# Optimization experiments

Measured on AMD Instinct MI355X. Metric: run time of the kernel, lower is better.

## Reference

```python
import jax, jax.numpy as jnp
import numpy as np


def silu(v):
    return v * jax.nn.sigmoid(v)


def setup_inputs() -> dict:
    key = jax.random.key(0)
    ks = jax.random.split(key, 9)
    B, L, d_model = 2, 2048, 1024
    expand, d_state, d_conv = 2, 16, 4
    d_inner = expand * d_model          # 2048
    dt_rank = (d_model + 15) // 16      # 64 (ceil(d_model/16))
    sc = 0.02
    s = lambda k, shape: (jax.random.normal(k, shape, jnp.float32) * sc)
    A_init = jnp.tile(jnp.arange(1, d_state + 1, dtype=jnp.float32), (d_inner, 1))
    return {
        "x": jax.random.normal(ks[0], (B, L, d_model), jnp.float32),
        "in_proj_w": s(ks[1], (2 * d_inner, d_model)),
        "conv_w": s(ks[2], (d_inner, 1, d_conv)),
        "conv_b": s(ks[3], (d_inner,)),
        "x_proj_w": s(ks[4], (dt_rank + 2 * d_state, d_inner)),
        "dt_proj_w": s(ks[5], (d_inner, dt_rank)),
        "dt_proj_b": s(ks[6], (d_inner,)),
        "A_log": jnp.log(A_init),
        "D": jnp.ones((d_inner,), jnp.float32),
        "out_proj_w": s(ks[7], (d_model, d_inner)),
    }


def _mamba(x, in_proj_w, conv_w, conv_b, x_proj_w, dt_proj_w, dt_proj_b, A_log, D, out_proj_w):
    Bsz, L, d_model = x.shape
    d_inner, _, d_conv = conv_w.shape
    d_state = A_log.shape[1]
    dt_rank = dt_proj_w.shape[1]

    # input projection -> [B, L, 2*d_inner], split into conv branch and gate
    xz = jnp.einsum('bld,ed->ble', x, in_proj_w)
    x_in, z = jnp.split(xz, 2, axis=-1)

    # causal depthwise conv1d over sequence
    xt = jnp.transpose(x_in, (0, 2, 1))                      # [B, d_inner, L]
    xt = jnp.pad(xt, ((0, 0), (0, 0), (d_conv - 1, 0)))
    xc = jax.lax.conv_general_dilated(
        xt, conv_w, window_strides=(1,), padding='VALID',
        dimension_numbers=('NCH', 'OIH', 'NCH'),
        feature_group_count=d_inner)
    xc = xc + conv_b[None, :, None]
    u = silu(jnp.transpose(xc, (0, 2, 1)))                   # [B, L, d_inner]

    # ssm parameter projections
    x_dbl = jnp.einsum('ble,fe->blf', u, x_proj_w)           # [B, L, dt_rank + 2*d_state]
    dt, B_ssm, C_ssm = jnp.split(x_dbl, [dt_rank, dt_rank + d_state], axis=-1)
    delta = jax.nn.softplus(jnp.einsum('blr,er->ble', dt, dt_proj_w) + dt_proj_b)  # [B,L,d_inner]
    A = -jnp.exp(A_log)                                       # [d_inner, d_state]

    # selective scan: h_t = exp(delta_t * A) * h_{t-1} + delta_t * u_t * B_t
    def step(h, inp):
        d_t, B_t, C_t, u_t = inp                              # [B,e],[B,n],[B,n],[B,e]
        dA = jnp.exp(d_t[..., None] * A)                      # [B, d_inner, d_state]
        h = dA * h + (d_t * u_t)[..., None] * B_t[:, None, :]
        y = jnp.einsum('ben,bn->be', h, C_t)
        return h, y

    h0 = jnp.zeros((Bsz, d_inner, d_state), x.dtype)
    scan_in = (jnp.swapaxes(delta, 0, 1), jnp.swapaxes(B_ssm, 0, 1),
               jnp.swapaxes(C_ssm, 0, 1), jnp.swapaxes(u, 0, 1))
    _, ys = jax.lax.scan(step, h0, scan_in)                   # ys: [L, B, d_inner]
    y = jnp.swapaxes(ys, 0, 1) + u * D                        # skip term D*u

    y = y * silu(z)                                           # gate
    return jnp.einsum('ble,de->bld', y, out_proj_w)


def reference(x, in_proj_w, conv_w, conv_b, x_proj_w, dt_proj_w, dt_proj_b, A_log, D, out_proj_w):
    # ResidualMamba: x + Mamba(x)
    return x + _mamba(x, in_proj_w, conv_w, conv_b, x_proj_w,
                      dt_proj_w, dt_proj_b, A_log, D, out_proj_w)
```

## Files before the change

kernel.cpp:

```cpp
#include <hip/hip_runtime.h>
#include <hip/hip_bf16.h>
#include <math.h>

typedef __bf16 bf16;
typedef __attribute__((ext_vector_type(8))) __bf16 bf16x8;
typedef __attribute__((ext_vector_type(4))) __bf16 bf16x4;
typedef __attribute__((ext_vector_type(4))) float  f32x4;

static constexpr int Bsz = 2, L = 2048, DM = 1024, DI = 2048, DS = 16, DTR = 64;
static constexpr int M   = Bsz * L;
static constexpr int NXZ = 2 * DI;
static constexpr int NXD = DTR + 2 * DS;
static constexpr int NC  = 32;
static constexpr int CL  = L / NC;
static constexpr int KS  = 8;
static constexpr float LOG2E = 1.4426950408889634f;

__device__ inline float ex2(float x) { return __builtin_amdgcn_exp2f(x); }

__device__ inline void gload_lds16(const void* g, void* l)
{
    __builtin_amdgcn_global_load_lds(
        (const __attribute__((address_space(1))) void*)g,
        (__attribute__((address_space(3))) void*)l, 16, 0, 0);
}

#define SBAR() { asm volatile("" ::: "memory"); __builtin_amdgcn_s_barrier(); asm volatile("" ::: "memory"); }
#define VMCNT4() asm volatile("s_waitcnt vmcnt(4)" ::: "memory")
#define VMCNT0() asm volatile("s_waitcnt vmcnt(0)" ::: "memory")

static constexpr int C0 = M * DM / 4;
static constexpr int C1 = C0 + NXZ * DM / 4;
static constexpr int C2 = C1 + DM * DI / 4;
static constexpr int C3 = C2 + NXD * DI / 4;
static constexpr int C4 = C3 + DI * DTR / 4;

__global__ __launch_bounds__(256)
void cast_all(const float* __restrict__ s0, const float* __restrict__ s1,
              const float* __restrict__ s2, const float* __restrict__ s3,
              const float* __restrict__ s4,
              bf16* __restrict__ d0, bf16* __restrict__ d1,
              bf16* __restrict__ d2, bf16* __restrict__ d3,
              bf16* __restrict__ d4)
{
    const int i = blockIdx.x * 256 + threadIdx.x;
    const float* s; bf16* d; int off;
    if      (i < C0) { s = s0; d = d0; off = 0;  }
    else if (i < C1) { s = s1; d = d1; off = C0; }
    else if (i < C2) { s = s2; d = d2; off = C1; }
    else if (i < C3) { s = s3; d = d3; off = C2; }
    else             { s = s4; d = d4; off = C3; }
    const int j = i - off;
    float4 v = ((const float4*)s)[j];
    bf16x4 o = {(bf16)v.x, (bf16)v.y, (bf16)v.z, (bf16)v.w};
    ((bf16x4*)d)[j] = o;
}

static constexpr int GK  = DM;
static constexpr int GNT = GK / 64;

__device__ __forceinline__ void stage_half(const bf16* __restrict__ Gbase, int ld,
                                           int kbase, bf16* lds_slot, int tid, int wid)
{
    const int rl = tid >> 2;
    const int ks = ((tid & 3) ^ (rl & 3)) << 3;
#pragma unroll
    for (int i = 0; i < 2; ++i)
        gload_lds16(Gbase + (size_t)(i * 128 + rl) * ld + kbase + ks,
                    lds_slot + i * 4096 + wid * 512);
}

template<int MH>
__device__ __forceinline__ void ldA4(const bf16* As, int abase, bf16x8 af[4])
{
#pragma unroll
    for (int mm = 0; mm < 4; ++mm)
        af[mm] = *(const bf16x8*)(As + abase + (MH * 4 + mm) * 512);
}

__device__ __forceinline__ void ldB4(const bf16* Bs, int bbase, bf16x8 bfr[4])
{
#pragma unroll
    for (int nn = 0; nn < 4; ++nn)
        bfr[nn] = *(const bf16x8*)(Bs + bbase + nn * 512);
}

template<int MH>
__device__ __forceinline__ void mfma16(f32x4 acc[8][4], const bf16x8 af[4],
                                       const bf16x8 bfr[4])
{
#pragma unroll
    for (int mm = 0; mm < 4; ++mm)
#pragma unroll
        for (int nn = 0; nn < 4; ++nn)
            acc[MH * 4 + mm][nn] = __builtin_amdgcn_mfma_f32_16x16x32_bf16(
                af[mm], bfr[nn], acc[MH * 4 + mm][nn], 0, 0, 0);
}

__global__ __launch_bounds__(512, 1)
void gemm256_inproj(const bf16* __restrict__ A, const bf16* __restrict__ Bw,
                    bf16* __restrict__ C)
{
    __shared__ __align__(16) bf16 Asl[4 * 8192];
    __shared__ __align__(16) bf16 Bsl[4 * 8192];

    const int tid  = threadIdx.x;
    const int wid  = tid >> 6;
    const int lane = tid & 63;
    const int wr   = wid >> 2;
    const int wc   = wid & 3;
    const int fr   = lane & 15;
    const int ko16 = lane >> 4;
    const int kx   = ((ko16 ^ (fr & 3)) << 3);

    const int bid = blockIdx.x;
    const int wg  = (bid & 7) * 32 + (bid >> 3);
    const int by  = wg >> 4, bx = wg & 15;
    const int row0 = by * 256, col0 = bx * 256;

    const bf16* Ablk = A  + (size_t)row0 * GK;
    const bf16* Bblk = Bw + (size_t)col0 * GK;

    const int abase = (wr * 128 + fr) * 32 + kx;
    const int bbase = (wc * 64 + fr) * 32 + kx;

    f32x4 acc[8][4] = {};
    bf16x8 af[4], bfr[4];

    stage_half(Ablk, GK, 0,       Asl + 0 * 8192, tid, wid);
    stage_half(Bblk, GK, 0,       Bsl + 0 * 8192, tid, wid);
    stage_half(Ablk, GK, 32,      Asl + 1 * 8192, tid, wid);
    stage_half(Bblk, GK, 32,      Bsl + 1 * 8192, tid, wid);
    stage_half(Ablk, GK, 64,      Asl + 2 * 8192, tid, wid);
    stage_half(Bblk, GK, 64,      Bsl + 2 * 8192, tid, wid);
    VMCNT4();
    SBAR();

    for (int t = 0; t < GNT; ++t) {
        const int sk0 = (2 * t) & 3, sk1 = (2 * t + 1) & 3;
        const bf16* As0 = Asl + sk0 * 8192;
        const bf16* As1 = Asl + sk1 * 8192;
        const bf16* Bs0 = Bsl + sk0 * 8192;
        const bf16* Bs1 = Bsl + sk1 * 8192;

        ldA4<0>(As0, abase, af);
        ldB4(Bs0, bbase, bfr);
        if (t + 1 < GNT)
            stage_half(Ablk, GK, (t + 1) * 64 + 32, Asl + ((2 * t + 3) & 3) * 8192, tid, wid);
        SBAR();
        __builtin_amdgcn_s_setprio(1);
        mfma16<0>(acc, af, bfr);
        __builtin_amdgcn_s_setprio(0);
        SBAR();

        ldA4<1>(As0, abase, af);
        if (t + 1 < GNT)
            stage_half(Bblk, GK, (t + 1) * 64 + 32, Bsl + ((2 * t + 3) & 3) * 8192, tid, wid);
        SBAR();
        __builtin_amdgcn_s_setprio(1);
        mfma16<1>(acc, af, bfr);
        __builtin_amdgcn_s_setprio(0);
        SBAR();

        ldA4<0>(As1, abase, af);
        ldB4(Bs1, bbase, bfr);
        if (t + 2 < GNT)
            stage_half(Ablk, GK, (t + 2) * 64, Asl + sk0 * 8192, tid, wid);
        SBAR();
        __builtin_amdgcn_s_setprio(1);
        mfma16<0>(acc, af, bfr);
        __builtin_amdgcn_s_setprio(0);
        SBAR();

        ldA4<1>(As1, abase, af);
        if (t + 2 < GNT)
            stage_half(Bblk, GK, (t + 2) * 64, Bsl + sk0 * 8192, tid, wid);
        SBAR();
        __builtin_amdgcn_s_setprio(1);
        mfma16<1>(acc, af, bfr);
        __builtin_amdgcn_s_setprio(0);
        if (t < GNT - 3) { VMCNT4(); } else { VMCNT0(); }
        SBAR();
    }

    const int r0 = row0 + wr * 128 + (ko16 << 2);
    const int c0 = col0 + wc * 64 + fr;
#pragma unroll
    for (int m = 0; m < 8; ++m)
#pragma unroll
        for (int n = 0; n < 4; ++n)
#pragma unroll
            for (int r = 0; r < 4; ++r)
                C[(size_t)(r0 + m * 16 + r) * NXZ + c0 + n * 16] = (bf16)acc[m][n][r];
}

__global__ __launch_bounds__(256)
void gemm_out(const bf16* __restrict__ A, const bf16* __restrict__ Bw,
              const float* __restrict__ res, float* __restrict__ Cout)
{
    __shared__ __align__(16) bf16 Asl[128 * 32];
    __shared__ __align__(16) bf16 Bsl[64 * 32];

    const int tid  = threadIdx.x;
    const int bid  = blockIdx.x;
    const int orig = (bid & 7) * 64 + (bid >> 3);
    const int bx   = orig & 15;
    const int by   = orig >> 4;
    const int row0 = by * 128, col0 = bx * 64;

    const int w    = tid >> 6;
    const int lane = tid & 63;
    const int wr   = w >> 1, wc = w & 1;
    const int fr   = lane & 15;
    const int ko   = (lane >> 4) << 3;

    f32x4 acc[4][2] = {};

    const int sr = tid >> 2;
    const int sk = (tid & 3) << 3;
    const bf16* gA0 = A  + (size_t)(row0 + sr) * NXZ + sk;
    const bf16* gA1 = A  + (size_t)(row0 + 64 + sr) * NXZ + sk;
    const bf16* gB0 = Bw + (size_t)(col0 + sr) * DI + sk;
    char* lA = (char*)Asl + w * 1024;
    char* lB = (char*)Bsl + w * 1024;

    for (int k0 = 0; k0 < DI; k0 += 32) {
        gload_lds16(gA0 + k0, lA);
        gload_lds16(gA1 + k0, lA + 4096);
        gload_lds16(gB0 + k0, lB);
        __syncthreads();

        bf16x8 af[4], bfr[2];
#pragma unroll
        for (int m = 0; m < 4; ++m)
            af[m] = *(const bf16x8*)&Asl[((wr << 6) + m * 16 + fr) * 32 + ko];
#pragma unroll
        for (int n = 0; n < 2; ++n)
            bfr[n] = *(const bf16x8*)&Bsl[((wc << 5) + n * 16 + fr) * 32 + ko];
#pragma unroll
        for (int m = 0; m < 4; ++m)
#pragma unroll
            for (int n = 0; n < 2; ++n)
                acc[m][n] = __builtin_amdgcn_mfma_f32_16x16x32_bf16(
                    af[m], bfr[n], acc[m][n], 0, 0, 0);
        __syncthreads();
    }

    const int r0 = row0 + (wr << 6) + ((lane >> 4) << 2);
    const int c0 = col0 + (wc << 5) + fr;
#pragma unroll
    for (int m = 0; m < 4; ++m)
#pragma unroll
        for (int n = 0; n < 2; ++n)
#pragma unroll
            for (int r = 0; r < 4; ++r) {
                const int row = r0 + m * 16 + r;
                const int col = c0 + n * 16;
                Cout[(size_t)row * DM + col] =
                    acc[m][n][r] + res[(size_t)row * DM + col];
            }
}

template<int EPI>
__global__ __launch_bounds__(256)
void gemm_bf16(const bf16* __restrict__ A, const bf16* __restrict__ Bw,
               const float* __restrict__ bias, const float* __restrict__ res,
               void* __restrict__ Cout, int N, int K, int lda, int ldc)
{
    __shared__ __align__(16) bf16 Asl[128 * 32];
    __shared__ __align__(16) bf16 Bsl[128 * 32];

    const int tid  = threadIdx.x;
    const int row0 = blockIdx.y * 128;
    const int col0 = blockIdx.x * 128;
    const int w    = tid >> 6;
    const int lane = tid & 63;
    const int wr   = w >> 1, wc = w & 1;
    const int fr   = lane & 15;
    const int ko   = (lane >> 4) << 3;

    f32x4 acc[4][4] = {};

    const int sr = tid >> 2;
    const int sk = (tid & 3) << 3;
    int brow0 = col0 + sr;       if (brow0 > N - 1) brow0 = N - 1;
    int brow1 = col0 + 64 + sr;  if (brow1 > N - 1) brow1 = N - 1;
    const bf16* gA0 = A  + (size_t)(row0 + sr) * lda + sk;
    const bf16* gA1 = A  + (size_t)(row0 + 64 + sr) * lda + sk;
    const bf16* gB0 = Bw + (size_t)brow0 * K + sk;
    const bf16* gB1 = Bw + (size_t)brow1 * K + sk;
    char* lA = (char*)Asl + w * 1024;
    char* lB = (char*)Bsl + w * 1024;

    for (int k0 = 0; k0 < K; k0 += 32) {
        gload_lds16(gA0 + k0, lA);
        gload_lds16(gA1 + k0, lA + 4096);
        gload_lds16(gB0 + k0, lB);
        gload_lds16(gB1 + k0, lB + 4096);
        __syncthreads();

        bf16x8 af[4], bfr[4];
#pragma unroll
        for (int m = 0; m < 4; ++m)
            af[m] = *(const bf16x8*)&Asl[((wr << 6) + m * 16 + fr) * 32 + ko];
#pragma unroll
        for (int n = 0; n < 4; ++n)
            bfr[n] = *(const bf16x8*)&Bsl[((wc << 6) + n * 16 + fr) * 32 + ko];
#pragma unroll
        for (int m = 0; m < 4; ++m)
#pragma unroll
            for (int n = 0; n < 4; ++n)
                acc[m][n] = __builtin_amdgcn_mfma_f32_16x16x32_bf16(
                    af[m], bfr[n], acc[m][n], 0, 0, 0);
        __syncthreads();
    }

    const int r0 = row0 + (wr << 6) + ((lane >> 4) << 2);
    const int c0 = col0 + (wc << 6) + fr;
#pragma unroll
    for (int m = 0; m < 4; ++m) {
#pragma unroll
        for (int n = 0; n < 4; ++n) {
            const int col = c0 + n * 16;
            if (col < N) {
#pragma unroll
                for (int r = 0; r < 4; ++r) {
                    const int row = r0 + m * 16 + r;
                    float v = acc[m][n][r];
                    if (EPI == 1) {
                        v += bias[col];
                        v = (v > 20.f) ? v : log1pf(expf(v));
                        ((bf16*)Cout)[(size_t)row * ldc + col] = (bf16)v;
                    } else {
                        ((bf16*)Cout)[(size_t)row * ldc + col] = (bf16)v;
                    }
                }
            }
        }
    }
}

__global__ __launch_bounds__(256)
void gemm_xproj(const bf16* __restrict__ A, const bf16* __restrict__ Bw,
                float* __restrict__ Cpart)
{
    __shared__ __align__(16) bf16 Asl[128 * 32];
    __shared__ __align__(16) bf16 Bsl[128 * 32];

    const int tid  = threadIdx.x;
    const int row0 = blockIdx.x * 128;
    const int kz   = blockIdx.y;
    const int kb   = kz * (2048 / KS);
    const int w    = tid >> 6;
    const int lane = tid & 63;
    const int wr   = w >> 1, wc = w & 1;
    const int fr   = lane & 15;
    const int ko   = (lane >> 4) << 3;

    f32x4 acc[4][4] = {};

    const int sr = tid >> 2;
    const int sk = (tid & 3) << 3;
    int brow0 = sr;       if (brow0 > 95) brow0 = 95;
    int brow1 = 64 + sr;  if (brow1 > 95) brow1 = 95;
    const bf16* gA0 = A  + (size_t)(row0 + sr) * DI + kb + sk;
    const bf16* gA1 = A  + (size_t)(row0 + 64 + sr) * DI + kb + sk;
    const bf16* gB0 = Bw + (size_t)brow0 * DI + kb + sk;
    const bf16* gB1 = Bw + (size_t)brow1 * DI + kb + sk;
    char* lA = (char*)Asl + w * 1024;
    char* lB = (char*)Bsl + w * 1024;

    for (int k0 = 0; k0 < 2048 / KS; k0 += 32) {
        gload_lds16(gA0 + k0, lA);
        gload_lds16(gA1 + k0, lA + 4096);
        gload_lds16(gB0 + k0, lB);
        gload_lds16(gB1 + k0, lB + 4096);
        __syncthreads();

        bf16x8 af[4], bfr[4];
#pragma unroll
        for (int m = 0; m < 4; ++m)
            af[m] = *(const bf16x8*)&Asl[((wr << 6) + m * 16 + fr) * 32 + ko];
#pragma unroll
        for (int n = 0; n < 4; ++n)
            bfr[n] = *(const bf16x8*)&Bsl[((wc << 6) + n * 16 + fr) * 32 + ko];
#pragma unroll
        for (int m = 0; m < 4; ++m)
#pragma unroll
            for (int n = 0; n < 4; ++n)
                acc[m][n] = __builtin_amdgcn_mfma_f32_16x16x32_bf16(
                    af[m], bfr[n], acc[m][n], 0, 0, 0);
        __syncthreads();
    }

    const int r0 = (wr << 6) + ((lane >> 4) << 2);
    const int c0 = (wc << 6) + fr;
    float* Cp = Cpart + (size_t)kz * M * 96 + (size_t)row0 * 96;
#pragma unroll
    for (int m = 0; m < 4; ++m) {
#pragma unroll
        for (int n = 0; n < 4; ++n) {
            const int col = c0 + n * 16;
            if (col < 96) {
#pragma unroll
                for (int r = 0; r < 4; ++r)
                    Cp[(size_t)(r0 + m * 16 + r) * 96 + col] = acc[m][n][r];
            }
        }
    }
}

__global__ __launch_bounds__(256)
void reduce_xdbl(const float* __restrict__ part, bf16* __restrict__ xdb)
{
    const int i = blockIdx.x * 256 + threadIdx.x;
    if (i >= M * 96) return;
    float s = 0.f;
#pragma unroll
    for (int k = 0; k < KS; ++k) s += part[(size_t)k * M * 96 + i];
    xdb[i] = (bf16)s;
}

__global__ __launch_bounds__(256)
void conv_silu(const bf16* __restrict__ xzb, const float* __restrict__ cw,
               const float* __restrict__ cb, bf16* __restrict__ u)
{
    const int idx = blockIdx.x * 256 + threadIdx.x;
    const int e   = (idx & 255) * 8;
    const int m   = idx >> 8;
    const int l   = m & (L - 1);

    float wv[8][4];
#pragma unroll
    for (int c = 0; c < 8; ++c) {
        float4 t = *(const float4*)(cw + (size_t)(e + c) * 4);
        wv[c][0] = t.x; wv[c][1] = t.y; wv[c][2] = t.z; wv[c][3] = t.w;
    }
    float acc[8];
    {
        float4 b0 = *(const float4*)(cb + e);
        float4 b1 = *(const float4*)(cb + e + 4);
        acc[0] = b0.x; acc[1] = b0.y; acc[2] = b0.z; acc[3] = b0.w;
        acc[4] = b1.x; acc[5] = b1.y; acc[6] = b1.z; acc[7] = b1.w;
    }
#pragma unroll
    for (int k = 0; k < 4; ++k) {
        if (l + k - 3 >= 0) {
            bf16x8 xv = *(const bf16x8*)&xzb[(size_t)(m + k - 3) * NXZ + e];
#pragma unroll
            for (int c = 0; c < 8; ++c)
                acc[c] = fmaf((float)xv[c], wv[c][k], acc[c]);
        }
    }
    bf16x8 o;
#pragma unroll
    for (int c = 0; c < 8; ++c)
        o[c] = (bf16)(acc[c] / (1.f + __expf(-acc[c])));
    *(bf16x8*)&u[(size_t)m * DI + e] = o;
}

__global__ __launch_bounds__(256)
void scan_pass1(const bf16* __restrict__ xzb, const bf16* __restrict__ ub,
                const bf16* __restrict__ xdb, const float* __restrict__ A_log,
                float* __restrict__ Pend, float* __restrict__ Qend)
{
    __shared__ bf16 sD[CL][256];
    __shared__ bf16 sU[CL][256];
    __shared__ float Bs[CL][DS];
    const int tid = threadIdx.x;
    const int e0 = blockIdx.x * 256;
    const int e  = e0 + tid;
    const int c = blockIdx.y;
    const int b = blockIdx.z;
    const int l0 = c * CL;

#pragma unroll
    for (int it = 0; it < CL / 8; ++it) {
        const int r   = it * 8 + (tid >> 5);
        const int col = (tid & 31) * 8;
        *(bf16x8*)&sD[r][col] = *(const bf16x8*)&xzb[(size_t)(b * L + l0 + r) * NXZ + e0 + col];
        *(bf16x8*)&sU[r][col] = *(const bf16x8*)&ub [(size_t)(b * L + l0 + r) * DI  + e0 + col];
    }
#pragma unroll
    for (int it = 0; it < CL * DS / 256; ++it) {
        const int idx = it * 256 + tid;
        Bs[idx >> 4][idx & 15] =
            (float)xdb[(size_t)(b * L + l0 + (idx >> 4)) * NXD + DTR + (idx & 15)];
    }

    float A2[DS];
#pragma unroll
    for (int q = 0; q < 4; ++q) {
        float4 al = *(const float4*)(A_log + (size_t)e * DS + q * 4);
        A2[q * 4 + 0] = -__expf(al.x) * LOG2E;
        A2[q * 4 + 1] = -__expf(al.y) * LOG2E;
        A2[q * 4 + 2] = -__expf(al.z) * LOG2E;
        A2[q * 4 + 3] = -__expf(al.w) * LOG2E;
    }

    float h[DS];
#pragma unroll
    for (int n = 0; n < DS; ++n) h[n] = 0.f;
    float sumd = 0.f;

    __syncthreads();

#pragma unroll 4
    for (int t = 0; t < CL; ++t) {
        const float dv = (float)sD[t][tid];
        const float uv = (float)sU[t][tid];
        const float du = dv * uv;
        sumd += dv;
#pragma unroll
        for (int n = 0; n < DS; ++n) {
            const float a = ex2(dv * A2[n]);
            h[n] = fmaf(a, h[n], du * Bs[t][n]);
        }
    }

    const size_t o = ((size_t)(c * Bsz + b) * DI + e) * DS;
#pragma unroll
    for (int q = 0; q < 4; ++q) {
        f32x4 P = {ex2(A2[q*4] * sumd), ex2(A2[q*4+1] * sumd),
                   ex2(A2[q*4+2] * sumd), ex2(A2[q*4+3] * sumd)};
        *(f32x4*)(Pend + o + q * 4) = P;
        *(float4*)(Qend + o + q * 4) = make_float4(h[q*4], h[q*4+1], h[q*4+2], h[q*4+3]);
    }
}

__global__ __launch_bounds__(256)
void scan_pass2(const float* __restrict__ Pend, const float* __restrict__ Qend,
                float* __restrict__ H0)
{
    const int g = blockIdx.x * 256 + threadIdx.x;
    const int stride = Bsz * DI * DS;
    float P[NC], Q[NC];
#pragma unroll
    for (int c = 0; c < NC; ++c) {
        P[c] = Pend[(size_t)c * stride + g];
        Q[c] = Qend[(size_t)c * stride + g];
    }
    float h = 0.f;
#pragma unroll
    for (int c = 0; c < NC; ++c) {
        H0[(size_t)c * stride + g] = h;
        h = fmaf(P[c], h, Q[c]);
    }
}

__global__ __launch_bounds__(256)
void scan_pass3(bf16* __restrict__ xzb, const bf16* __restrict__ ub,
                const bf16* __restrict__ xdb, const float* __restrict__ A_log,
                const float* __restrict__ Dp, const float* __restrict__ H0)
{
    __shared__ bf16 sD[CL][256];
    __shared__ bf16 sU[CL][256];
    __shared__ float BCs[CL][2 * DS];
    const int tid = threadIdx.x;
    const int e0 = blockIdx.x * 256;
    const int e  = e0 + tid;
    const int c = blockIdx.y;
    const int b = blockIdx.z;
    const int l0 = c * CL;

#pragma unroll
    for (int it = 0; it < CL / 8; ++it) {
        const int r   = it * 8 + (tid >> 5);
        const int col = (tid & 31) * 8;
        const size_t grow = (size_t)(b * L + l0 + r);
        *(bf16x8*)&sD[r][col] = *(const bf16x8*)&xzb[grow * NXZ + e0 + col];
        *(bf16x8*)&sU[r][col] = *(const bf16x8*)&ub [grow * DI + e0 + col];
    }
#pragma unroll
    for (int it = 0; it < CL * 2 * DS / 256; ++it) {
        const int idx = it * 256 + tid;
        BCs[idx >> 5][idx & 31] =
            (float)xdb[(size_t)(b * L + l0 + (idx >> 5)) * NXD + DTR + (idx & 31)];
    }

    float A2[DS];
#pragma unroll
    for (int q = 0; q < 4; ++q) {
        float4 al = *(const float4*)(A_log + (size_t)e * DS + q * 4);
        A2[q * 4 + 0] = -__expf(al.x) * LOG2E;
        A2[q * 4 + 1] = -__expf(al.y) * LOG2E;
        A2[q * 4 + 2] = -__expf(al.z) * LOG2E;
        A2[q * 4 + 3] = -__expf(al.w) * LOG2E;
    }

    float h[DS];
    const size_t o = (size_t)c * (Bsz * DI * DS) + ((size_t)b * DI + e) * DS;
#pragma unroll
    for (int q = 0; q < 4; ++q) {
        float4 hv = *(const float4*)(H0 + o + q * 4);
        h[q*4] = hv.x; h[q*4+1] = hv.y; h[q*4+2] = hv.z; h[q*4+3] = hv.w;
    }
    const float Dval = Dp[e];

    __syncthreads();

#pragma unroll 4
    for (int t = 0; t < CL; ++t) {
        const float dv = (float)sD[t][tid];
        const float uv = (float)sU[t][tid];
        const float du = dv * uv;
        float y = 0.f;
#pragma unroll
        for (int n = 0; n < DS; ++n) {
            const float a = ex2(dv * A2[n]);
            h[n] = fmaf(a, h[n], du * BCs[t][n]);
            y = fmaf(h[n], BCs[t][DS + n], y);
        }
        sD[t][tid] = (bf16)(y + uv * Dval);
    }

    __syncthreads();
#pragma unroll
    for (int it = 0; it < CL / 8; ++it) {
        const int r   = it * 8 + (tid >> 5);
        const int col = (tid & 31) * 8;
        const size_t grow = (size_t)(b * L + l0 + r);
        bf16x8 zv = *(const bf16x8*)&xzb[grow * NXZ + DI + e0 + col];
        bf16x8 yv = *(bf16x8*)&sD[r][col];
        bf16x8 ov;
#pragma unroll
        for (int j = 0; j < 8; ++j) {
            const float z = (float)zv[j];
            ov[j] = (bf16)((float)yv[j] * (z / (1.f + __expf(-z))));
        }
        *(bf16x8*)&xzb[grow * NXZ + e0 + col] = ov;
    }
}

extern "C" void kernel_launch(void* const* d_in, const int* in_sizes, int n_in,
                              void* d_out, int out_size, void* d_ws, size_t ws_size,
                              hipStream_t stream)
{
    const float* x          = (const float*)d_in[0];
    const float* in_proj_w  = (const float*)d_in[1];
    const float* conv_w     = (const float*)d_in[2];
    const float* conv_b     = (const float*)d_in[3];
    const float* x_proj_w   = (const float*)d_in[4];
    const float* dt_proj_w  = (const float*)d_in[5];
    const float* dt_proj_b  = (const float*)d_in[6];
    const float* A_log      = (const float*)d_in[7];
    const float* Dp         = (const float*)d_in[8];
    const float* out_proj_w = (const float*)d_in[9];
    float* out = (float*)d_out;

    bf16* xzb   = (bf16*)d_ws;
    bf16* ub    = xzb   + (size_t)M * NXZ;
    bf16* xdb   = ub    + (size_t)M * DI;
    bf16* xb    = xdb   + (size_t)M * NXD;
    bf16* wbin  = xb    + (size_t)M * DM;
    bf16* wbout = wbin  + (size_t)NXZ * DM;
    bf16* wbxp  = wbout + (size_t)DM * DI;
    bf16* wbdt  = wbxp  + (size_t)NXD * DI;
    float* Pend = (float*)(wbdt + (size_t)DI * DTR);
    float* Qend = Pend + (size_t)NC * Bsz * DI * DS;
    float* H0   = Qend + (size_t)NC * Bsz * DI * DS;
    float* xpart = Pend;

    const dim3 blk(256);

    cast_all<<<dim3(C4 / 256), blk, 0, stream>>>(
        x, in_proj_w, out_proj_w, x_proj_w, dt_proj_w,
        xb, wbin, wbout, wbxp, wbdt);

    gemm256_inproj<<<dim3(256), dim3(512), 0, stream>>>(xb, wbin, xzb);

    conv_silu<<<dim3(M * (DI / 8) / 256), blk, 0, stream>>>(xzb, conv_w, conv_b, ub);

    gemm_xproj<<<dim3(M / 128, KS), blk, 0, stream>>>(ub, wbxp, xpart);
    reduce_xdbl<<<dim3(M * 96 / 256), blk, 0, stream>>>(xpart, xdb);

    gemm_bf16<1><<<dim3(DI / 128, M / 128), blk, 0, stream>>>(
        xdb, wbdt, dt_proj_b, nullptr, xzb, DI, DTR, NXD, NXZ);

    scan_pass1<<<dim3(DI / 256, NC, Bsz), blk, 0, stream>>>(xzb, ub, xdb, A_log, Pend, Qend);
    scan_pass2<<<dim3(Bsz * DI * DS / 256), blk, 0, stream>>>(Pend, Qend, H0);
    scan_pass3<<<dim3(DI / 256, NC, Bsz), blk, 0, stream>>>(xzb, ub, xdb, A_log, Dp, H0);

    gemm_out<<<dim3(512), blk, 0, stream>>>(xzb, wbout, x, out);
}
```

Baseline: 246.7 us.

## Re-swizzle LDS layout in GEMMs and double-buffer gemm_out k-loop

Changes the LDS swizzle pattern from XOR-based to a rotation based on row bits in all GEMM kernels, so that the 16-byte fragment reads conflict less across banks. gemm_out gains double-buffered LDS staging: the next k-slice is issued before computing on the current one, with vmcnt waits and raised wave priority around the MFMAs. This aims to hide global-load latency and cut bank conflicts, at the cost of twice the LDS in gemm_out and an extra barrier per iteration.

```diff
diff --git a/kernel.cpp b/kernel.cpp
--- a/kernel.cpp
+++ b/kernel.cpp
@@ -27,7 +27,9 @@
 
 #define SBAR() { asm volatile("" ::: "memory"); __builtin_amdgcn_s_barrier(); asm volatile("" ::: "memory"); }
 #define VMCNT4() asm volatile("s_waitcnt vmcnt(4)" ::: "memory")
+#define VMCNT3() asm volatile("s_waitcnt vmcnt(3)" ::: "memory")
 #define VMCNT0() asm volatile("s_waitcnt vmcnt(0)" ::: "memory")
+
 
 static constexpr int C0 = M * DM / 4;
 static constexpr int C1 = C0 + NXZ * DM / 4;
@@ -63,7 +65,7 @@
                                            int kbase, bf16* lds_slot, int tid, int wid)
 {
     const int rl = tid >> 2;
-    const int ks = ((tid & 3) ^ (rl & 3)) << 3;
+    const int ks = ((((tid & 3) - ((tid >> 3) & 3)) & 3) << 3);
 #pragma unroll
     for (int i = 0; i < 2; ++i)
         gload_lds16(Gbase + (size_t)(i * 128 + rl) * ld + kbase + ks,
@@ -111,7 +113,7 @@
     const int wc   = wid & 3;
     const int fr   = lane & 15;
     const int ko16 = lane >> 4;
-    const int kx   = ((ko16 ^ (fr & 3)) << 3);
+    const int kx   = (((ko16 + ((fr >> 1) & 3)) & 3) << 3);
 
     const int bid = blockIdx.x;
     const int wg  = (bid & 7) * 32 + (bid >> 3);
@@ -198,8 +200,8 @@
 void gemm_out(const bf16* __restrict__ A, const bf16* __restrict__ Bw,
               const float* __restrict__ res, float* __restrict__ Cout)
 {
-    __shared__ __align__(16) bf16 Asl[128 * 32];
-    __shared__ __align__(16) bf16 Bsl[64 * 32];
+    __shared__ __align__(16) bf16 Asl[2][128 * 32];
+    __shared__ __align__(16) bf16 Bsl[2][64 * 32];
 
     const int tid  = threadIdx.x;
     const int bid  = blockIdx.x;
@@ -212,39 +214,50 @@
     const int lane = tid & 63;
     const int wr   = w >> 1, wc = w & 1;
     const int fr   = lane & 15;
-    const int ko   = (lane >> 4) << 3;
+    const int ko   = (((lane >> 4) + ((fr >> 1) & 3)) & 3) << 3;
 
     f32x4 acc[4][2] = {};
 
-    const int sr = tid >> 2;
-    const int sk = (tid & 3) << 3;
-    const bf16* gA0 = A  + (size_t)(row0 + sr) * NXZ + sk;
-    const bf16* gA1 = A  + (size_t)(row0 + 64 + sr) * NXZ + sk;
-    const bf16* gB0 = Bw + (size_t)(col0 + sr) * DI + sk;
-    char* lA = (char*)Asl + w * 1024;
-    char* lB = (char*)Bsl + w * 1024;
-
+    const int sr  = tid >> 2;
+    const int ssk = ((((tid & 3) - ((tid >> 3) & 3)) & 3) << 3);
+    const bf16* gA0 = A  + (size_t)(row0 + sr) * NXZ + ssk;
+    const bf16* gA1 = A  + (size_t)(row0 + 64 + sr) * NXZ + ssk;
+    const bf16* gB0 = Bw + (size_t)(col0 + sr) * DI + ssk;
+
+#define STAGE_OUT(s, kk) do { \
+        gload_lds16(gA0 + (kk), (char*)Asl[s] + w * 1024); \
+        gload_lds16(gA1 + (kk), (char*)Asl[s] + 4096 + w * 1024); \
+        gload_lds16(gB0 + (kk), (char*)Bsl[s] + w * 1024); } while (0)
+
+    STAGE_OUT(0, 0);
     for (int k0 = 0; k0 < DI; k0 += 32) {
-        gload_lds16(gA0 + k0, lA);
-        gload_lds16(gA1 + k0, lA + 4096);
-        gload_lds16(gB0 + k0, lB);
-        __syncthreads();
+        const int cur = (k0 >> 5) & 1;
+        if (k0 + 32 < DI) {
+            STAGE_OUT(cur ^ 1, k0 + 32);
+            VMCNT3();
+        } else {
+            VMCNT0();
+        }
+        SBAR();
 
         bf16x8 af[4], bfr[2];
 #pragma unroll
         for (int m = 0; m < 4; ++m)
-            af[m] = *(const bf16x8*)&Asl[((wr << 6) + m * 16 + fr) * 32 + ko];
+            af[m] = *(const bf16x8*)&Asl[cur][((wr << 6) + m * 16 + fr) * 32 + ko];
 #pragma unroll
         for (int n = 0; n < 2; ++n)
-            bfr[n] = *(const bf16x8*)&Bsl[((wc << 5) + n * 16 + fr) * 32 + ko];
+            bfr[n] = *(const bf16x8*)&Bsl[cur][((wc << 5) + n * 16 + fr) * 32 + ko];
+        __builtin_amdgcn_s_setprio(1);
 #pragma unroll
         for (int m = 0; m < 4; ++m)
 #pragma unroll
             for (int n = 0; n < 2; ++n)
                 acc[m][n] = __builtin_amdgcn_mfma_f32_16x16x32_bf16(
                     af[m], bfr[n], acc[m][n], 0, 0, 0);
-        __syncthreads();
-    }
+        __builtin_amdgcn_s_setprio(0);
+        SBAR();
+    }
+#undef STAGE_OUT
 
     const int r0 = row0 + (wr << 6) + ((lane >> 4) << 2);
     const int c0 = col0 + (wc << 5) + fr;
@@ -277,18 +290,18 @@
     const int lane = tid & 63;
     const int wr   = w >> 1, wc = w & 1;
     const int fr   = lane & 15;
-    const int ko   = (lane >> 4) << 3;
+    const int ko   = (((lane >> 4) + ((fr >> 1) & 3)) & 3) << 3;
 
     f32x4 acc[4][4] = {};
 
-    const int sr = tid >> 2;
-    const int sk = (tid & 3) << 3;
+    const int sr  = tid >> 2;
+    const int ssk = ((((tid & 3) - ((tid >> 3) & 3)) & 3) << 3);
     int brow0 = col0 + sr;       if (brow0 > N - 1) brow0 = N - 1;
     int brow1 = col0 + 64 + sr;  if (brow1 > N - 1) brow1 = N - 1;
-    const bf16* gA0 = A  + (size_t)(row0 + sr) * lda + sk;
-    const bf16* gA1 = A  + (size_t)(row0 + 64 + sr) * lda + sk;
-    const bf16* gB0 = Bw + (size_t)brow0 * K + sk;
-    const bf16* gB1 = Bw + (size_t)brow1 * K + sk;
+    const bf16* gA0 = A  + (size_t)(row0 + sr) * lda + ssk;
+    const bf16* gA1 = A  + (size_t)(row0 + 64 + sr) * lda + ssk;
+    const bf16* gB0 = Bw + (size_t)brow0 * K + ssk;
+    const bf16* gB1 = Bw + (size_t)brow1 * K + ssk;
     char* lA = (char*)Asl + w * 1024;
     char* lB = (char*)Bsl + w * 1024;
 
@@ -355,18 +368,18 @@
     const int lane = tid & 63;
     const int wr   = w >> 1, wc = w & 1;
     const int fr   = lane & 15;
-    const int ko   = (lane >> 4) << 3;
+    const int ko   = (((lane >> 4) + ((fr >> 1) & 3)) & 3) << 3;
 
     f32x4 acc[4][4] = {};
 
-    const int sr = tid >> 2;
-    const int sk = (tid & 3) << 3;
+    const int sr  = tid >> 2;
+    const int ssk = ((((tid & 3) - ((tid >> 3) & 3)) & 3) << 3);
     int brow0 = sr;       if (brow0 > 95) brow0 = 95;
     int brow1 = 64 + sr;  if (brow1 > 95) brow1 = 95;
-    const bf16* gA0 = A  + (size_t)(row0 + sr) * DI + kb + sk;
-    const bf16* gA1 = A  + (size_t)(row0 + 64 + sr) * DI + kb + sk;
-    const bf16* gB0 = Bw + (size_t)brow0 * DI + kb + sk;
-    const bf16* gB1 = Bw + (size_t)brow1 * DI + kb + sk;
+    const bf16* gA0 = A  + (size_t)(row0 + sr) * DI + kb + ssk;
+    const bf16* gA1 = A  + (size_t)(row0 + 64 + sr) * DI + kb + ssk;
+    const bf16* gB0 = Bw + (size_t)brow0 * DI + kb + ssk;
+    const bf16* gB1 = Bw + (size_t)brow1 * DI + kb + ssk;
     char* lA = (char*)Asl + w * 1024;
     char* lB = (char*)Bsl + w * 1024;
 
```

Measured after the change: 245.2 us, median of 2. No clear change (-0.6%).
